# Performance work log

Measured on AMD Instinct MI355X. Metric: run time of the kernel, lower is better.

## Reference

```python
import jax, jax.numpy as jnp
import numpy as np

# Architecture dims (from setArch args)
B, IN = 256, 1024          # batch, inputSize
E, H1, S = 32, 1024, 512   # numStateEnsembles, stateHiddenLayerSize, stateEnsembleOutputSize
H2, F = 512, 64            # featureHiddenLayerSize, numStateFeatures
NO, HO, OF = 16, 512, 1    # numOutputEnsembles, outputEnsembleHiddenLayerSize, outputEnsembleFeatures
T = E * F                  # thalamusSpaceSize
TIN = IN + T               # totalInputSize


def setup_inputs() -> dict:
    key = jax.random.key(0)
    ks = jax.random.split(key, 14)
    sc = 0.02
    f32 = jnp.float32
    return {
        "inputs": jax.random.normal(ks[0], (B, IN), f32),
        # stacked state-ensemble params: Linear(TIN,H1) -> Softplus -> Linear(H1,S)
        "sw1": jax.random.normal(ks[1], (E, TIN, H1), f32) * sc,
        "sb1": jax.random.normal(ks[2], (E, H1), f32) * sc,
        "sw2": jax.random.normal(ks[3], (E, H1, S), f32) * sc,
        "sb2": jax.random.normal(ks[4], (E, S), f32) * sc,
        # stacked feature-ensemble params: Linear(S,H2) -> ReLU -> Linear(H2,F)
        "fw1": jax.random.normal(ks[5], (E, S, H2), f32) * sc,
        "fb1": jax.random.normal(ks[6], (E, H2), f32) * sc,
        "fw2": jax.random.normal(ks[7], (E, H2, F), f32) * sc,
        "fb2": jax.random.normal(ks[8], (E, F), f32) * sc,
        # stacked output-ensemble params: Linear(S+1,HO) -> ReLU -> Linear(HO,OF)
        "ow1": jax.random.normal(ks[9], (NO, S + 1, HO), f32) * sc,
        "ob1": jax.random.normal(ks[10], (NO, HO), f32) * sc,
        "ow2": jax.random.normal(ks[11], (NO, HO, OF), f32) * sc,
        "ob2": jax.random.normal(ks[12], (NO, OF), f32) * sc,
        "action": 1,
        "context": 3,
        "num_iterations": 4,
    }


def reference(inputs, sw1, sb1, sw2, sb2, fw1, fb1, fw2, fb2,
              ow1, ob1, ow2, ob2, action, context, num_iterations):
    b = inputs.shape[0]
    # resetThalamus: savedThalamusFeatures = zeros(E*F)
    thal = jnp.zeros((b, T), inputs.dtype)
    state = None
    for _ in range(num_iterations):
        # leInput = cat(thalamusFeatures, inputs)  -> [B, TIN]
        x = jnp.concatenate([thal, inputs], axis=-1)
        # all E state ensembles batched: Linear -> Softplus -> Linear
        h = jax.nn.softplus(jnp.einsum('bi,eih->beh', x, sw1) + sb1)   # [B,E,H1]
        state = jnp.einsum('beh,ehs->bes', h, sw2) + sb2               # [B,E,S]
        # all E feature ensembles batched: Linear -> ReLU -> Linear
        g = jax.nn.relu(jnp.einsum('bes,esh->beh', state, fw1) + fb1)  # [B,E,H2]
        feat = jnp.einsum('beh,ehf->bef', g, fw2) + fb2                # [B,E,F]
        # thalamusFeatures = concatenate(computedFeatures)
        thal = feat.reshape(b, T)
    # output ensemble for `context` on cat([action], stateValues[context])
    sc_state = state[:, context, :]                                    # [B,S]
    a = jnp.full((b, 1), action, inputs.dtype)
    y = jnp.concatenate([a, sc_state], axis=-1)                        # [B,S+1]
    z = jax.nn.relu(y @ ow1[context] + ob1[context])                   # [B,HO]
    reward = z @ ow2[context] + ob2[context]                           # [B,OF]
    return reward
```

## Files before the change

kernel.cpp:

```cpp
#include <hip/hip_runtime.h>
#include <hip/hip_bf16.h>

#define B_SZ 256
#define IN_  1024
#define E_   32
#define H1_  1024
#define S_   512
#define H2_  512
#define F_   64
#define T_   2048
#define TIN_ 3072
#define NO_  16
#define HO_  512

typedef __attribute__((ext_vector_type(8))) short bf16x8;
typedef __attribute__((ext_vector_type(4))) float f32x4;

__device__ __forceinline__ unsigned short f2bf(float f) {
    unsigned u = __builtin_bit_cast(unsigned, f);
    u += 0x7fffu + ((u >> 16) & 1u);
    return (unsigned short)(u >> 16);
}
__device__ __forceinline__ float bf2f(unsigned short h) {
    return __builtin_bit_cast(float, ((unsigned)h) << 16);
}
__device__ __forceinline__ float softplusf(float x) {
    return fmaxf(x, 0.0f) + log1pf(expf(-fabsf(x)));
}
__device__ __forceinline__ void gload_lds16(const void* g, void* l) {
    __builtin_amdgcn_global_load_lds(
        (const __attribute__((address_space(1))) unsigned int*)g,
        (__attribute__((address_space(3))) unsigned int*)l,
        16, 0, 0);
}

__global__ __launch_bounds__(256) void cvt_t64(const float* __restrict__ in,
                                               unsigned short* __restrict__ out,
                                               int K, int N) {
    __shared__ float tile[64][65];
    const size_t eoff = (size_t)blockIdx.z * K * N;
    const float* ip = in + eoff;
    unsigned short* op = out + eoff;
    const int k0 = blockIdx.x * 64, n0 = blockIdx.y * 64;
    const int t = threadIdx.x;
    const int lr = t >> 4;
    const int lc = (t & 15) << 2;
    #pragma unroll
    for (int i = 0; i < 4; ++i) {
        const float4 v = *(const float4*)&ip[(size_t)(k0 + lr + 16 * i) * N + n0 + lc];
        float* dst = &tile[lr + 16 * i][lc];
        dst[0] = v.x; dst[1] = v.y; dst[2] = v.z; dst[3] = v.w;
    }
    __syncthreads();
    #pragma unroll
    for (int i = 0; i < 4; ++i) {
        const int n = (t >> 4) + 16 * i;
        const int k = (t & 15) << 2;
        ushort4 o;
        o.x = f2bf(tile[k][n]); o.y = f2bf(tile[k + 1][n]);
        o.z = f2bf(tile[k + 2][n]); o.w = f2bf(tile[k + 3][n]);
        *(ushort4*)&op[(size_t)(n0 + n) * K + k0 + k] = o;
    }
}

__global__ void x_init(const float* __restrict__ inp, unsigned short* __restrict__ x) {
    const int i = blockIdx.x * 256 + threadIdx.x;
    const int b = i / (IN_ / 4), c = (i % (IN_ / 4)) * 4;
    const float4 v = *(const float4*)&inp[(size_t)b * IN_ + c];
    ushort4 o;
    o.x = f2bf(v.x); o.y = f2bf(v.y); o.z = f2bf(v.z); o.w = f2bf(v.w);
    *(ushort4*)&x[(size_t)b * TIN_ + T_ + c] = o;
}

template<int BM, int BN, int TPB, int WMT, int WNT, int ACT, int ADD_BASE, int OUTM, bool PAIRED>
__global__ __launch_bounds__(TPB) void gemm_k(
    const unsigned short* __restrict__ A, int lda, long strideAe,
    int kOff, int K,
    const unsigned short* __restrict__ W, int ldw, long strideWe,
    const float* __restrict__ bias,
    const unsigned short* __restrict__ baseBuf,
    void* __restrict__ out, void* __restrict__ out2,
    int ldc, long strideOe, int N)
{
    constexpr int MI = BM / (16 * WMT), NI = BN / (16 * WNT);
    constexpr int AL = (BM * 4) / TPB, BL = (BN * 4) / TPB;
    __shared__ unsigned short As0[BM * 32], Bs0[BN * 32];
    __shared__ unsigned short As1[BM * 32], Bs1[BN * 32];

    int e, m0, n0;
    if constexpr (PAIRED) {
        const int bid = blockIdx.x;
        const int NBn = N / BN;
        m0 = (bid >> 8) * BM;
        const int rem = bid & 255;
        n0 = (rem % NBn) * BN;
        e  = rem / NBn;
    } else {
        e = blockIdx.z; m0 = blockIdx.x * BM; n0 = blockIdx.y * BN;
    }

    const int tid = threadIdx.x;
    const int wid = tid >> 6;
    const int lane = tid & 63;
    const int wm = wid / WNT, wn = wid % WNT;
    const unsigned short* Ae = A + (size_t)e * strideAe + (size_t)m0 * lda + kOff;
    const unsigned short* We = W + (size_t)e * strideWe + (size_t)n0 * ldw + kOff;

    f32x4 acc[MI][NI];
    #pragma unroll
    for (int i = 0; i < MI; ++i)
        #pragma unroll
        for (int j = 0; j < NI; ++j) {
            f32x4 z = {0.f, 0.f, 0.f, 0.f};
            acc[i][j] = z;
        }
    const int lr = lane & 15;
    const int lk = (lane >> 4) << 3;

    auto stage = [&](unsigned short* Asb, unsigned short* Bsb, int kt) {
        const int kk = kt * 32;
        #pragma unroll
        for (int p = 0; p < AL; ++p) {
            const int seg = p * TPB + tid;
            const int r = seg >> 2, cc = (seg & 3) << 3;
            gload_lds16(Ae + (size_t)r * lda + kk + cc, Asb + ((size_t)(p * TPB + wid * 64)) * 8);
        }
        #pragma unroll
        for (int p = 0; p < BL; ++p) {
            const int seg = p * TPB + tid;
            const int r = seg >> 2, cc = (seg & 3) << 3;
            gload_lds16(We + (size_t)r * ldw + kk + cc, Bsb + ((size_t)(p * TPB + wid * 64)) * 8);
        }
    };
    auto compute = [&](const unsigned short* Asb, const unsigned short* Bsb) {
        bf16x8 af2[MI], bfv[NI];
        #pragma unroll
        for (int mi = 0; mi < MI; ++mi)
            af2[mi] = *(const bf16x8*)&Asb[(wm * MI * 16 + mi * 16 + lr) * 32 + lk];
        #pragma unroll
        for (int ni = 0; ni < NI; ++ni)
            bfv[ni] = *(const bf16x8*)&Bsb[(wn * NI * 16 + ni * 16 + lr) * 32 + lk];
        #pragma unroll
        for (int mi = 0; mi < MI; ++mi)
            #pragma unroll
            for (int ni = 0; ni < NI; ++ni)
                acc[mi][ni] = __builtin_amdgcn_mfma_f32_16x16x32_bf16(
                    af2[mi], bfv[ni], acc[mi][ni], 0, 0, 0);
    };

    const int nt = K / 32;
    stage(As0, Bs0, 0);
    __syncthreads();
    for (int t = 0; t < nt; t += 2) {
        stage(As1, Bs1, t + 1);
        compute(As0, Bs0);
        __syncthreads();
        if (t + 2 < nt) stage(As0, Bs0, t + 2);
        compute(As1, Bs1);
        __syncthreads();
    }

    const int lg = lane >> 4;
    #pragma unroll
    for (int ni = 0; ni < NI; ++ni) {
        const int col = n0 + wn * NI * 16 + ni * 16 + lr;
        const float bv = bias ? bias[(size_t)e * N + col] : 0.0f;
        #pragma unroll
        for (int mi = 0; mi < MI; ++mi) {
            #pragma unroll
            for (int r = 0; r < 4; ++r) {
                const int row = m0 + wm * MI * 16 + mi * 16 + lg * 4 + r;
                float v = acc[mi][ni][r] + bv;
                if constexpr (ADD_BASE) v += bf2f(baseBuf[((size_t)e * B_SZ + row) * H1_ + col]);
                if constexpr (ACT == 1) v = softplusf(v);
                if constexpr (ACT == 2) v = fmaxf(v, 0.0f);
                const size_t oidx = (size_t)e * strideOe + (size_t)row * ldc + col;
                if constexpr (OUTM == 2) {
                    ((unsigned short*)out)[oidx] = f2bf(v);
                    ((unsigned short*)out2)[oidx] = f2bf(softplusf(v));
                } else {
                    ((unsigned short*)out)[oidx] = f2bf(v);
                }
            }
        }
    }
    (void)out2;
}

__global__ __launch_bounds__(512) void head_z(const unsigned short* __restrict__ state,
                                              const float* __restrict__ ow1,
                                              const float* __restrict__ ob1,
                                              const int* __restrict__ actp,
                                              const int* __restrict__ ctxp,
                                              float* __restrict__ z) {
    __shared__ float ys[16][516];
    const int ctx = *ctxp;
    const float act = (float)(*actp);
    const int b0 = blockIdx.x * 16;
    const int t = threadIdx.x;
    for (int bb = 0; bb < 16; ++bb)
        ys[bb][1 + t] = bf2f(state[((size_t)(ctx * B_SZ + b0 + bb)) * S_ + t]);
    if (t < 16) ys[t][0] = act;
    __syncthreads();
    const float* w = ow1 + (size_t)ctx * (S_ + 1) * HO_;
    float acc[16];
    #pragma unroll
    for (int bb = 0; bb < 16; ++bb) acc[bb] = 0.0f;
    for (int k = 0; k < S_ + 1; ++k) {
        const float wv = w[(size_t)k * HO_ + t];
        #pragma unroll
        for (int bb = 0; bb < 16; ++bb) acc[bb] += ys[bb][k] * wv;
    }
    const float b1 = ob1[ctx * HO_ + t];
    for (int bb = 0; bb < 16; ++bb)
        z[(size_t)(b0 + bb) * HO_ + t] = fmaxf(acc[bb] + b1, 0.0f);
}

__global__ void head_r(const float* __restrict__ z, const float* __restrict__ ow2,
                       const float* __restrict__ ob2, const int* __restrict__ ctxp,
                       float* __restrict__ out) {
    const int ctx = *ctxp;
    const int b = blockIdx.x;
    const int t = threadIdx.x;
    const float* w = ow2 + (size_t)ctx * HO_;
    float s = 0.0f;
    for (int h = t; h < HO_; h += 64) s += z[(size_t)b * HO_ + h] * w[h];
    #pragma unroll
    for (int off = 32; off; off >>= 1) s += __shfl_down(s, off);
    if (t == 0) out[b] = s + ob2[ctx];
}

extern "C" void kernel_launch(void* const* d_in, const int* in_sizes, int n_in,
                              void* d_out, int out_size, void* d_ws, size_t ws_size,
                              hipStream_t stream) {
    (void)in_sizes; (void)n_in; (void)out_size; (void)ws_size;
    const float* inputs = (const float*)d_in[0];
    const float* sw1 = (const float*)d_in[1];
    const float* sb1 = (const float*)d_in[2];
    const float* sw2 = (const float*)d_in[3];
    const float* sb2 = (const float*)d_in[4];
    const float* fw1 = (const float*)d_in[5];
    const float* fb1 = (const float*)d_in[6];
    const float* fw2 = (const float*)d_in[7];
    const float* fb2 = (const float*)d_in[8];
    const float* ow1 = (const float*)d_in[9];
    const float* ob1 = (const float*)d_in[10];
    const float* ow2 = (const float*)d_in[11];
    const float* ob2 = (const float*)d_in[12];
    const int* actp = (const int*)d_in[13];
    const int* ctxp = (const int*)d_in[14];

    char* p = (char*)d_ws;
    unsigned short* w1t = (unsigned short*)p; p += (size_t)E_ * H1_ * TIN_ * 2;
    unsigned short* w2t = (unsigned short*)p; p += (size_t)E_ * S_ * H1_ * 2;
    unsigned short* f1t = (unsigned short*)p; p += (size_t)E_ * H2_ * S_ * 2;
    unsigned short* f2t = (unsigned short*)p; p += (size_t)E_ * F_ * H2_ * 2;
    unsigned short* xbf = (unsigned short*)p; p += (size_t)B_SZ * TIN_ * 2;
    unsigned short* base = (unsigned short*)p; p += (size_t)E_ * B_SZ * H1_ * 2;
    unsigned short* hbf = (unsigned short*)p; p += (size_t)E_ * B_SZ * H1_ * 2;
    unsigned short* stbf = (unsigned short*)p; p += (size_t)E_ * B_SZ * S_ * 2;
    unsigned short* gbf = (unsigned short*)p; p += (size_t)E_ * B_SZ * H2_ * 2;
    float* zbuf = (float*)p;                  p += (size_t)B_SZ * HO_ * 4;

    cvt_t64<<<dim3(TIN_ / 64, H1_ / 64, E_), 256, 0, stream>>>(sw1, w1t, TIN_, H1_);
    cvt_t64<<<dim3(H1_ / 64, S_ / 64, E_),  256, 0, stream>>>(sw2, w2t, H1_, S_);
    cvt_t64<<<dim3(S_ / 64, H2_ / 64, E_),  256, 0, stream>>>(fw1, f1t, S_, H2_);
    cvt_t64<<<dim3(H2_ / 64, F_ / 64, E_),  256, 0, stream>>>(fw2, f2t, H2_, F_);
    x_init<<<(B_SZ * IN_ / 4) / 256, 256, 0, stream>>>(inputs, xbf);

    gemm_k<128, 128, 512, 2, 4, 0, 0, 2, true><<<dim3(512), 512, 0, stream>>>(
        xbf, TIN_, 0L, T_, IN_, w1t, TIN_, (long)H1_ * TIN_, sb1, nullptr,
        base, hbf, H1_, (long)B_SZ * H1_, H1_);

    for (int it = 0; it < 4; ++it) {
        if (it > 0) {
            gemm_k<128, 128, 512, 2, 4, 1, 1, 0, true><<<dim3(512), 512, 0, stream>>>(
                xbf, TIN_, 0L, 0, T_, w1t, TIN_, (long)H1_ * TIN_, nullptr, base,
                hbf, nullptr, H1_, (long)B_SZ * H1_, H1_);
        }
        gemm_k<128, 64, 256, 2, 2, 0, 0, 0, true><<<dim3(512), 256, 0, stream>>>(
            hbf, H1_, (long)B_SZ * H1_, 0, H1_, w2t, H1_, (long)S_ * H1_, sb2, nullptr,
            stbf, nullptr, S_, (long)B_SZ * S_, S_);
        if (it < 3) {
            gemm_k<128, 64, 256, 2, 2, 2, 0, 0, true><<<dim3(512), 256, 0, stream>>>(
                stbf, S_, (long)B_SZ * S_, 0, S_, f1t, S_, (long)H2_ * S_, fb1, nullptr,
                gbf, nullptr, H2_, (long)B_SZ * H2_, H2_);
            gemm_k<64, 64, 256, 2, 2, 0, 0, 0, false><<<dim3(4, 1, E_), 256, 0, stream>>>(
                gbf, H2_, (long)B_SZ * H2_, 0, H2_, f2t, H2_, (long)F_ * H2_, fb2, nullptr,
                xbf, nullptr, TIN_, 64L, F_);
        }
    }
    head_z<<<B_SZ / 16, 512, 0, stream>>>(stbf, ow1, ob1, actp, ctxp, zbuf);
    head_r<<<B_SZ, 64, 0, stream>>>(zbuf, ow2, ob2, ctxp, (float*)d_out);
}
```

Baseline: 744.5 us.

## Merge weight conversions, fuse output head, retile first-layer GEMMs to 256x64

Merges the four weight-transpose/convert launches into one kernel and fuses the two output-head kernels, so the intermediate z buffer and its launch go away. The big first-layer GEMMs switch from paired 128x128 tiles with 512 threads to 256x64 tiles with 256 threads. Each block then covers the whole batch, so every weight tile is read once per ensemble. It also adds a minimum-occupancy hint of four blocks to launch_bounds. The new tiling and occupancy hint may raise register pressure or change how efficiently the MFMA units are used.

```diff
diff --git a/kernel.cpp b/kernel.cpp
--- a/kernel.cpp
+++ b/kernel.cpp
@@ -34,14 +34,23 @@
         16, 0, 0);
 }
 
-__global__ __launch_bounds__(256) void cvt_t64(const float* __restrict__ in,
-                                               unsigned short* __restrict__ out,
-                                               int K, int N) {
+__global__ __launch_bounds__(256) void cvt_all(
+    const float* __restrict__ sw1, const float* __restrict__ sw2,
+    const float* __restrict__ fw1, const float* __restrict__ fw2,
+    unsigned short* __restrict__ w1t, unsigned short* __restrict__ w2t,
+    unsigned short* __restrict__ f1t, unsigned short* __restrict__ f2t)
+{
     __shared__ float tile[64][65];
-    const size_t eoff = (size_t)blockIdx.z * K * N;
+    const int bx = blockIdx.x, e = blockIdx.y;
+    const float* in; unsigned short* out; int K, N, kx, ny;
+    if (bx < 768)      { in = sw1; out = w1t; K = TIN_; N = H1_; kx = bx % 48;        ny = bx / 48; }
+    else if (bx < 896) { in = sw2; out = w2t; K = H1_;  N = S_;  kx = (bx-768) % 16;  ny = (bx-768) / 16; }
+    else if (bx < 960) { in = fw1; out = f1t; K = S_;   N = H2_; kx = (bx-896) % 8;   ny = (bx-896) / 8; }
+    else               { in = fw2; out = f2t; K = H2_;  N = F_;  kx = bx - 960;       ny = 0; }
+    const size_t eoff = (size_t)e * K * N;
     const float* ip = in + eoff;
     unsigned short* op = out + eoff;
-    const int k0 = blockIdx.x * 64, n0 = blockIdx.y * 64;
+    const int k0 = kx * 64, n0 = ny * 64;
     const int t = threadIdx.x;
     const int lr = t >> 4;
     const int lc = (t & 15) << 2;
@@ -73,7 +82,7 @@
 }
 
 template<int BM, int BN, int TPB, int WMT, int WNT, int ACT, int ADD_BASE, int OUTM, bool PAIRED>
-__global__ __launch_bounds__(TPB) void gemm_k(
+__global__ __launch_bounds__(TPB, 4) void gemm_k(
     const unsigned short* __restrict__ A, int lda, long strideAe,
     int kOff, int K,
     const unsigned short* __restrict__ W, int ldw, long strideWe,
@@ -187,13 +196,16 @@
     (void)out2;
 }
 
-__global__ __launch_bounds__(512) void head_z(const unsigned short* __restrict__ state,
-                                              const float* __restrict__ ow1,
-                                              const float* __restrict__ ob1,
-                                              const int* __restrict__ actp,
-                                              const int* __restrict__ ctxp,
-                                              float* __restrict__ z) {
+__global__ __launch_bounds__(512) void head(const unsigned short* __restrict__ state,
+                                            const float* __restrict__ ow1,
+                                            const float* __restrict__ ob1,
+                                            const float* __restrict__ ow2,
+                                            const float* __restrict__ ob2,
+                                            const int* __restrict__ actp,
+                                            const int* __restrict__ ctxp,
+                                            float* __restrict__ out) {
     __shared__ float ys[16][516];
+    __shared__ float part[16][9];
     const int ctx = *ctxp;
     const float act = (float)(*actp);
     const int b0 = blockIdx.x * 16;
@@ -203,31 +215,31 @@
     if (t < 16) ys[t][0] = act;
     __syncthreads();
     const float* w = ow1 + (size_t)ctx * (S_ + 1) * HO_;
-    float acc[16];
-    #pragma unroll
-    for (int bb = 0; bb < 16; ++bb) acc[bb] = 0.0f;
+    float accv[16];
+    #pragma unroll
+    for (int bb = 0; bb < 16; ++bb) accv[bb] = 0.0f;
     for (int k = 0; k < S_ + 1; ++k) {
         const float wv = w[(size_t)k * HO_ + t];
         #pragma unroll
-        for (int bb = 0; bb < 16; ++bb) acc[bb] += ys[bb][k] * wv;
+        for (int bb = 0; bb < 16; ++bb) accv[bb] += ys[bb][k] * wv;
     }
     const float b1 = ob1[ctx * HO_ + t];
-    for (int bb = 0; bb < 16; ++bb)
-        z[(size_t)(b0 + bb) * HO_ + t] = fmaxf(acc[bb] + b1, 0.0f);
-}
-
-__global__ void head_r(const float* __restrict__ z, const float* __restrict__ ow2,
-                       const float* __restrict__ ob2, const int* __restrict__ ctxp,
-                       float* __restrict__ out) {
-    const int ctx = *ctxp;
-    const int b = blockIdx.x;
-    const int t = threadIdx.x;
-    const float* w = ow2 + (size_t)ctx * HO_;
-    float s = 0.0f;
-    for (int h = t; h < HO_; h += 64) s += z[(size_t)b * HO_ + h] * w[h];
-    #pragma unroll
-    for (int off = 32; off; off >>= 1) s += __shfl_down(s, off);
-    if (t == 0) out[b] = s + ob2[ctx];
+    const float w2v = ow2[(size_t)ctx * HO_ + t];
+    const int lane = t & 63, wv8 = t >> 6;
+    #pragma unroll
+    for (int bb = 0; bb < 16; ++bb) {
+        float s = fmaxf(accv[bb] + b1, 0.0f) * w2v;
+        #pragma unroll
+        for (int off = 32; off; off >>= 1) s += __shfl_down(s, off);
+        if (lane == 0) part[bb][wv8] = s;
+    }
+    __syncthreads();
+    if (t < 16) {
+        float s = ob2[ctx];
+        #pragma unroll
+        for (int w8 = 0; w8 < 8; ++w8) s += part[t][w8];
+        out[b0 + t] = s;
+    }
 }
 
 extern "C" void kernel_launch(void* const* d_in, const int* in_sizes, int n_in,
@@ -260,21 +272,17 @@
     unsigned short* hbf = (unsigned short*)p; p += (size_t)E_ * B_SZ * H1_ * 2;
     unsigned short* stbf = (unsigned short*)p; p += (size_t)E_ * B_SZ * S_ * 2;
     unsigned short* gbf = (unsigned short*)p; p += (size_t)E_ * B_SZ * H2_ * 2;
-    float* zbuf = (float*)p;                  p += (size_t)B_SZ * HO_ * 4;
-
-    cvt_t64<<<dim3(TIN_ / 64, H1_ / 64, E_), 256, 0, stream>>>(sw1, w1t, TIN_, H1_);
-    cvt_t64<<<dim3(H1_ / 64, S_ / 64, E_),  256, 0, stream>>>(sw2, w2t, H1_, S_);
-    cvt_t64<<<dim3(S_ / 64, H2_ / 64, E_),  256, 0, stream>>>(fw1, f1t, S_, H2_);
-    cvt_t64<<<dim3(H2_ / 64, F_ / 64, E_),  256, 0, stream>>>(fw2, f2t, H2_, F_);
+
+    cvt_all<<<dim3(968, E_), 256, 0, stream>>>(sw1, sw2, fw1, fw2, w1t, w2t, f1t, f2t);
     x_init<<<(B_SZ * IN_ / 4) / 256, 256, 0, stream>>>(inputs, xbf);
 
-    gemm_k<128, 128, 512, 2, 4, 0, 0, 2, true><<<dim3(512), 512, 0, stream>>>(
+    gemm_k<256, 64, 256, 2, 2, 0, 0, 2, false><<<dim3(1, H1_ / 64, E_), 256, 0, stream>>>(
         xbf, TIN_, 0L, T_, IN_, w1t, TIN_, (long)H1_ * TIN_, sb1, nullptr,
         base, hbf, H1_, (long)B_SZ * H1_, H1_);
 
     for (int it = 0; it < 4; ++it) {
         if (it > 0) {
-            gemm_k<128, 128, 512, 2, 4, 1, 1, 0, true><<<dim3(512), 512, 0, stream>>>(
+            gemm_k<256, 64, 256, 2, 2, 1, 1, 0, false><<<dim3(1, H1_ / 64, E_), 256, 0, stream>>>(
                 xbf, TIN_, 0L, 0, T_, w1t, TIN_, (long)H1_ * TIN_, nullptr, base,
                 hbf, nullptr, H1_, (long)B_SZ * H1_, H1_);
         }
@@ -290,6 +298,5 @@
                 xbf, nullptr, TIN_, 64L, F_);
         }
     }
-    head_z<<<B_SZ / 16, 512, 0, stream>>>(stbf, ow1, ob1, actp, ctxp, zbuf);
-    head_r<<<B_SZ, 64, 0, stream>>>(zbuf, ow2, ob2, ctxp, (float*)d_out);
-}
+    head<<<B_SZ / 16, 512, 0, stream>>>(stbf, ow1, ob1, ow2, ob2, actp, ctxp, (float*)d_out);
+}
```

Result: slower. 984.8 us (+32.3%).
